# Optimization experiments

Hardware: AMD Instinct MI355X
Metric: run time of the kernel (lower is better)

Reference implementation:

```python
import jax, jax.numpy as jnp
import numpy as np

N_NODES = 100000
N_EDGES = 1600000
IN_CH = 128
EDGE_CH = 16
HEADS = 4
OUT_CH = 16


def setup_inputs() -> dict:
    key = jax.random.key(0)
    k1, k2, k3, k4, k5, k6, k7 = jax.random.split(key, 7)
    x = jax.random.normal(k1, (N_NODES, IN_CH), dtype=jnp.float32)
    edge_index = jax.random.randint(k2, (2, N_EDGES), 0, N_NODES, dtype=jnp.int64)
    edge_attr = jax.random.normal(k3, (N_EDGES, EDGE_CH), dtype=jnp.float32)
    W = jax.random.normal(k4, (IN_CH, HEADS * OUT_CH), dtype=jnp.float32) * 0.05
    W_edge = jax.random.normal(k5, (EDGE_CH, HEADS), dtype=jnp.float32) * 0.05
    a = jax.random.normal(k6, (HEADS, 2 * OUT_CH), dtype=jnp.float32) * 0.05
    return {"x": x, "edge_index": edge_index, "edge_attr": edge_attr,
            "W": W, "W_edge": W_edge, "a": a}


def reference(x, edge_index, edge_attr, W, W_edge, a):
    # x: [N, in_ch]; edge_index: [2, E]; edge_attr: [E, edge_ch]
    N = x.shape[0]
    H, twoC = a.shape
    C = twoC // 2
    row, col = edge_index[0], edge_index[1]

    h = (x @ W).reshape(N, H, C)                      # [N, H, C]
    # Split attention vector: score_e = sum(x_i * a_l) + sum(x_j * a_r)
    a_l, a_r = a[:, :C], a[:, C:]                     # [H, C] each
    alpha_l = jnp.einsum('nhc,hc->nh', h, a_l)        # [N, H] per-node left score
    alpha_r = jnp.einsum('nhc,hc->nh', h, a_r)        # [N, H] per-node right score

    alpha = alpha_l[row] + alpha_r[col]               # [E, H]
    alpha = alpha + edge_attr @ W_edge                # add edge scores [E, H]
    alpha = jnp.where(alpha > 0, alpha, 0.2 * alpha)  # LeakyReLU(0.2)

    # Segment softmax over destination node (col)
    amax = jax.ops.segment_max(alpha, col, num_segments=N)        # [N, H]
    ex = jnp.exp(alpha - amax[col])                                # [E, H]
    denom = jax.ops.segment_sum(ex, col, num_segments=N)           # [N, H]
    denom = jnp.clip(denom, 1e-10)
    alpha = ex / denom[col]                                        # [E, H]

    # Aggregate: out[n] = sum over edges with col==n of x_j * alpha
    x_j = h[col]                                                   # [E, H, C]
    out = jax.ops.segment_sum(x_j * alpha[..., None], col, num_segments=N)
    return out.reshape(N, H * C)
```

## Files before the change

kernel.cpp:

```cpp
#include <hip/hip_runtime.h>

typedef short short8 __attribute__((ext_vector_type(8)));
typedef float f32x4 __attribute__((ext_vector_type(4)));

#define KDIM 128
#define OUTW 64
#define WT_STRIDE 136
#define FLAG_SET ((unsigned char)0x5C)

__device__ __forceinline__ short f2bf(float f) {
    unsigned u = __float_as_uint(f);
    u += 0x7FFFu + ((u >> 16) & 1u);
    return (short)(u >> 16);
}

__global__ __launch_bounds__(256) void flag_bytes(const int* __restrict__ col,
                                                  unsigned char* __restrict__ flag,
                                                  int E, int N) {
    int i = blockIdx.x * 256 + threadIdx.x;
    int e0 = i * 4;
    if (e0 + 3 < E) {
        int4 c = *(const int4*)(col + e0);
        if ((unsigned)c.x < (unsigned)N) flag[c.x] = FLAG_SET;
        if ((unsigned)c.y < (unsigned)N) flag[c.y] = FLAG_SET;
        if ((unsigned)c.z < (unsigned)N) flag[c.z] = FLAG_SET;
        if ((unsigned)c.w < (unsigned)N) flag[c.w] = FLAG_SET;
    } else {
        for (int e = e0; e < E; ++e) {
            int c = col[e];
            if ((unsigned)c < (unsigned)N) flag[c] = FLAG_SET;
        }
    }
}

__global__ __launch_bounds__(256) void gemm_mfma(const float* __restrict__ x,
                                                 const float* __restrict__ W,
                                                 const unsigned char* __restrict__ flag,
                                                 float* __restrict__ out,
                                                 int N, int nStrips) {
    __shared__ __align__(16) short Wt[OUTW * WT_STRIDE];

    const int tid  = threadIdx.x;
    const int lane = tid & 63;
    const int wid  = tid >> 6;
    const int m    = lane & 15;
    const int q    = lane >> 4;

    for (int i = tid; i < KDIM * OUTW; i += 256) {
        int k = i >> 6;
        int c = i & 63;
        Wt[c * WT_STRIDE + k] = f2bf(W[i]);
    }
    __syncthreads();

    short8 bfrag[4][4];
    #pragma unroll
    for (int s = 0; s < 4; ++s)
        #pragma unroll
        for (int c = 0; c < 4; ++c)
            bfrag[s][c] = *(const short8*)&Wt[(c * 16 + m) * WT_STRIDE + s * 32 + q * 8];

    const int strip = blockIdx.x * 4 + wid;
    if (strip >= nStrips) return;
    const int base = strip * 16;
    const int arow = base + m;
    const float* xp = x + (size_t)arow * KDIM;

    f32x4 acc[4] = {f32x4{0,0,0,0}, f32x4{0,0,0,0}, f32x4{0,0,0,0}, f32x4{0,0,0,0}};

    #pragma unroll
    for (int s = 0; s < 4; ++s) {
        float4 f0 = make_float4(0.f, 0.f, 0.f, 0.f);
        float4 f1 = make_float4(0.f, 0.f, 0.f, 0.f);
        if (arow < N) {
            f0 = *(const float4*)(xp + s * 32 + q * 8);
            f1 = *(const float4*)(xp + s * 32 + q * 8 + 4);
        }
        short8 a;
        a[0] = f2bf(f0.x); a[1] = f2bf(f0.y); a[2] = f2bf(f0.z); a[3] = f2bf(f0.w);
        a[4] = f2bf(f1.x); a[5] = f2bf(f1.y); a[6] = f2bf(f1.z); a[7] = f2bf(f1.w);
        #pragma unroll
        for (int c = 0; c < 4; ++c)
            acc[c] = __builtin_amdgcn_mfma_f32_16x16x32_bf16(a, bfrag[s][c], acc[c], 0, 0, 0);
    }

    #pragma unroll
    for (int r = 0; r < 4; ++r) {
        int orow = base + q * 4 + r;
        if (orow < N) {
            float mv = (flag[orow] == FLAG_SET) ? 1.f : 0.f;
            float* op = out + (size_t)orow * OUTW + m;
            #pragma unroll
            for (int c = 0; c < 4; ++c)
                op[c * 16] = acc[c][r] * mv;
        }
    }
}

extern "C" void kernel_launch(void* const* d_in, const int* in_sizes, int n_in,
                              void* d_out, int out_size, void* d_ws, size_t ws_size,
                              hipStream_t stream) {
    const float* x  = (const float*)d_in[0];
    const int*   ei = (const int*)d_in[1];
    const float* W  = (const float*)d_in[3];
    float* out = (float*)d_out;

    const int N = in_sizes[0] / KDIM;
    const int E = in_sizes[1] / 2;
    const int* col = ei + E;

    unsigned char* flag = (unsigned char*)d_ws;

    const int fBlocks = ((E + 3) / 4 + 255) / 256;
    flag_bytes<<<fBlocks, 256, 0, stream>>>(col, flag, E, N);

    const int nStrips = (N + 15) / 16;
    const int blocks  = (nStrips + 3) / 4;
    gemm_mfma<<<blocks, 256, 0, stream>>>(x, W, flag, out, N, nStrips);
}
```

Baseline: 195.6 us.

## Fuse destination-flag scatter into GEMM kernel and zero unflagged rows in fixup pass

The edge-destination flag scatter now runs as a grid-stride loop at the start of the MFMA GEMM kernel, so its scattered byte stores overlap with GEMM work instead of running as a separate kernel first. The GEMM no longer reads the flag or applies a mask when storing rows. A small follow-up kernel reads the flags four at a time and zeroes the output rows of nodes with no incoming edges. This reorders the work across the two launches, but there are still two launches, and GEMM blocks now carry extra scatter work before their tile computation starts.

```diff
diff --git a/kernel.cpp b/kernel.cpp
--- a/kernel.cpp
+++ b/kernel.cpp
@@ -14,37 +14,34 @@
     return (short)(u >> 16);
 }
 
-__global__ __launch_bounds__(256) void flag_bytes(const int* __restrict__ col,
+__global__ __launch_bounds__(256) void fused_main(const float* __restrict__ x,
+                                                  const float* __restrict__ W,
+                                                  const int* __restrict__ col,
                                                   unsigned char* __restrict__ flag,
-                                                  int E, int N) {
-    int i = blockIdx.x * 256 + threadIdx.x;
-    int e0 = i * 4;
-    if (e0 + 3 < E) {
-        int4 c = *(const int4*)(col + e0);
-        if ((unsigned)c.x < (unsigned)N) flag[c.x] = FLAG_SET;
-        if ((unsigned)c.y < (unsigned)N) flag[c.y] = FLAG_SET;
-        if ((unsigned)c.z < (unsigned)N) flag[c.z] = FLAG_SET;
-        if ((unsigned)c.w < (unsigned)N) flag[c.w] = FLAG_SET;
-    } else {
-        for (int e = e0; e < E; ++e) {
-            int c = col[e];
-            if ((unsigned)c < (unsigned)N) flag[c] = FLAG_SET;
+                                                  float* __restrict__ out,
+                                                  int N, int E, int nStrips) {
+    __shared__ __align__(16) short Wt[OUTW * WT_STRIDE];
+
+    const int tid = threadIdx.x;
+
+    {
+        const int gt = blockIdx.x * 256 + tid;
+        const int stride4 = gridDim.x * 256 * 4;
+        for (int e0 = gt * 4; e0 < E; e0 += stride4) {
+            if (e0 + 3 < E) {
+                int4 c = *(const int4*)(col + e0);
+                if ((unsigned)c.x < (unsigned)N) flag[c.x] = FLAG_SET;
+                if ((unsigned)c.y < (unsigned)N) flag[c.y] = FLAG_SET;
+                if ((unsigned)c.z < (unsigned)N) flag[c.z] = FLAG_SET;
+                if ((unsigned)c.w < (unsigned)N) flag[c.w] = FLAG_SET;
+            } else {
+                for (int e = e0; e < E; ++e) {
+                    int c = col[e];
+                    if ((unsigned)c < (unsigned)N) flag[c] = FLAG_SET;
+                }
+            }
         }
     }
-}
-
-__global__ __launch_bounds__(256) void gemm_mfma(const float* __restrict__ x,
-                                                 const float* __restrict__ W,
-                                                 const unsigned char* __restrict__ flag,
-                                                 float* __restrict__ out,
-                                                 int N, int nStrips) {
-    __shared__ __align__(16) short Wt[OUTW * WT_STRIDE];
-
-    const int tid  = threadIdx.x;
-    const int lane = tid & 63;
-    const int wid  = tid >> 6;
-    const int m    = lane & 15;
-    const int q    = lane >> 4;
 
     for (int i = tid; i < KDIM * OUTW; i += 256) {
         int k = i >> 6;
@@ -52,6 +49,11 @@
         Wt[c * WT_STRIDE + k] = f2bf(W[i]);
     }
     __syncthreads();
+
+    const int lane = tid & 63;
+    const int wid  = tid >> 6;
+    const int m    = lane & 15;
+    const int q    = lane >> 4;
 
     short8 bfrag[4][4];
     #pragma unroll
@@ -88,11 +90,35 @@
     for (int r = 0; r < 4; ++r) {
         int orow = base + q * 4 + r;
         if (orow < N) {
-            float mv = (flag[orow] == FLAG_SET) ? 1.f : 0.f;
             float* op = out + (size_t)orow * OUTW + m;
             #pragma unroll
             for (int c = 0; c < 4; ++c)
-                op[c * 16] = acc[c][r] * mv;
+                op[c * 16] = acc[c][r];
+        }
+    }
+}
+
+__global__ __launch_bounds__(256) void fixup(const unsigned char* __restrict__ flag,
+                                             float* __restrict__ out, int N) {
+    int i4 = blockIdx.x * 256 + threadIdx.x;
+    int n0 = i4 * 4;
+    if (n0 >= N) return;
+    unsigned fv;
+    if (n0 + 3 < N) {
+        fv = *(const unsigned*)(flag + n0);
+    } else {
+        fv = 0;
+        for (int j = 0; j < 4; ++j)
+            if (n0 + j < N) fv |= (unsigned)flag[n0 + j] << (8 * j);
+    }
+    #pragma unroll
+    for (int j = 0; j < 4; ++j) {
+        int n = n0 + j;
+        if (n < N && (unsigned char)((fv >> (8 * j)) & 0xFFu) != FLAG_SET) {
+            float4 z = make_float4(0.f, 0.f, 0.f, 0.f);
+            float4* op = (float4*)(out + (size_t)n * OUTW);
+            #pragma unroll
+            for (int c = 0; c < OUTW / 4; ++c) op[c] = z;
         }
     }
 }
@@ -111,10 +137,10 @@
 
     unsigned char* flag = (unsigned char*)d_ws;
 
-    const int fBlocks = ((E + 3) / 4 + 255) / 256;
-    flag_bytes<<<fBlocks, 256, 0, stream>>>(col, flag, E, N);
-
     const int nStrips = (N + 15) / 16;
     const int blocks  = (nStrips + 3) / 4;
-    gemm_mfma<<<blocks, 256, 0, stream>>>(x, W, flag, out, N, nStrips);
+    fused_main<<<blocks, 256, 0, stream>>>(x, W, col, flag, out, N, E, nStrips);
+
+    const int fBlocks = ((N + 3) / 4 + 255) / 256;
+    fixup<<<fBlocks, 256, 0, stream>>>(flag, out, N);
 }
```

Result: no change. 192.3 us (-1.7%).
